# Performance work log

Measured on AMD Instinct MI355X. Metric: run time of the kernel, lower is better.

The kernel has to match this reference:

```python
import jax, jax.numpy as jnp
import numpy as np

T = 2048          # sequence length
B = 1             # batch (forced by out.squeeze(1))
H = 2048          # hidden_size == input_size
L = 2             # num_layers
V = 128           # num_letters
TEMPERATURE = 1.0


def _lstm_layer(x, h0, c0, W_ih, W_hh, b_ih, b_hh):
    # x: [T, B, H_in], h0/c0: [B, H], W_ih: [4H, H_in], W_hh: [4H, H]
    b = b_ih + b_hh

    def step(carry, x_t):
        h, c = carry
        gates = x_t @ W_ih.T + h @ W_hh.T + b            # [B, 4H]
        i, f, g, o = jnp.split(gates, 4, axis=-1)        # torch gate order i,f,g,o
        i = jax.nn.sigmoid(i)
        f = jax.nn.sigmoid(f)
        g = jnp.tanh(g)
        o = jax.nn.sigmoid(o)
        c = f * c + i * g
        h = o * jnp.tanh(c)
        return (h, c), h

    (hT, cT), ys = jax.lax.scan(step, (h0, c0), x)       # ys: [T, B, H]
    return ys, hT, cT


def setup_inputs() -> dict:
    key = jax.random.key(0)
    ks = jax.random.split(key, 10)
    s = 1.0 / np.sqrt(H)  # torch default uniform init bound
    u = lambda k, shape: jax.random.uniform(k, shape, jnp.float32, -s, s)
    return {
        "x": jax.random.normal(ks[0], (T, B, H), jnp.float32),
        "h0": jnp.zeros((L, B, H), jnp.float32),
        "c0": jnp.zeros((L, B, H), jnp.float32),
        "W_ih": u(ks[1], (L, 4 * H, H)),
        "W_hh": u(ks[2], (L, 4 * H, H)),
        "b_ih": u(ks[3], (L, 4 * H)),
        "b_hh": u(ks[4], (L, 4 * H)),
        "fc_w": u(ks[5], (V, H)),
        "fc_b": u(ks[6], (V,)),
    }


def reference(x, h0, c0, W_ih, W_hh, b_ih, b_hh, fc_w, fc_b):
    out = x
    h_n, c_n = [], []
    for l in range(L):  # fixed small layer loop (dropout=0.1 is identity in eval)
        out, hT, cT = _lstm_layer(out, h0[l], c0[l], W_ih[l], W_hh[l], b_ih[l], b_hh[l])
        h_n.append(hT)
        c_n.append(cT)
    h_n = jnp.stack(h_n)
    c_n = jnp.stack(c_n)
    logits = out[:, 0, :] @ fc_w.T + fc_b                 # squeeze(1) -> [T, V]
    logp = jax.nn.log_softmax(logits / TEMPERATURE, axis=1)
    return logp, (h_n, c_n)
```

## Files before the change

### kernel.cpp

```cpp
#include <hip/hip_runtime.h>
#include <hip/hip_fp16.h>

#define T_LEN 2048
#define HID   2048
#define G4    8192
#define NV    128

typedef _Float16 h2_t __attribute__((ext_vector_type(2)));
typedef unsigned u32x4 __attribute__((ext_vector_type(4)));

__device__ __forceinline__ float uplo(unsigned u) {
  return __half2float(__ushort_as_half((unsigned short)(u & 0xffffu)));
}
__device__ __forceinline__ float uphi(unsigned u) {
  return __half2float(__ushort_as_half((unsigned short)(u >> 16)));
}
__device__ __forceinline__ unsigned pku(float a, float b) {
  unsigned lo = (unsigned)__half_as_ushort(__float2half_rn(a));
  unsigned hi = (unsigned)__half_as_ushort(__float2half_rn(b));
  return lo | (hi << 16);
}
__device__ __forceinline__ h2_t pk2(float a, float bb) {
  return __builtin_bit_cast(h2_t, __builtin_amdgcn_cvt_pkrtz(a, bb));
}

__device__ __forceinline__ uint4 ld_sc16(const unsigned* p) {
  uint4 r;
  asm volatile("global_load_dwordx4 %0, %1, off sc0 sc1\n\ts_waitcnt vmcnt(0)"
               : "=v"(r) : "v"(p) : "memory");
  return r;
}
__device__ __forceinline__ void st_sc16(unsigned* p, u32x4 v) {
  asm volatile("global_store_dwordx4 %0, %1, off sc0 sc1\n\ts_waitcnt vmcnt(0)"
               :: "v"(p), "v"(v) : "memory");
}
__device__ __forceinline__ void st_sc4(unsigned* p, unsigned v) {
  asm volatile("global_store_dword %0, %1, off sc0 sc1"
               :: "v"(p), "v"(v) : "memory");
}

__device__ __forceinline__ float fsigmoid(float x) {
  return __builtin_amdgcn_rcpf(1.f + __expf(-x));
}
__device__ __forceinline__ float ftanh(float x) {
  return 2.f * __builtin_amdgcn_rcpf(1.f + __expf(-2.f * x)) - 1.f;
}

__device__ __forceinline__ void poll_flags(const unsigned* f, unsigned want,
                                           int lane) {
  const unsigned* p = f + 4 * lane;
  int sp = 0;
  for (;;) {
    uint4 u = ld_sc16(p);
    bool ok = (u.x == want) & (u.y == want) & (u.z == want) & (u.w == want);
    if (__all(ok)) break;
    if (++sp > 8) __builtin_amdgcn_s_sleep(1);
    if (sp > (1 << 15)) break;
  }
}

__global__ __launch_bounds__(256) void zero_flags(unsigned* f, int n4) {
  u32x4 z = {0u, 0u, 0u, 0u};
  for (int i = blockIdx.x * 256 + threadIdx.x; i < n4; i += gridDim.x * 256)
    st_sc16(f + 4 * (size_t)i, z);
}

__global__ __launch_bounds__(256, 2) void gemm_bias(
    const float* __restrict__ A, const float* __restrict__ B,
    const float* __restrict__ b1, const float* __restrict__ b2,
    float* __restrict__ C)
{
  const int N = 8192, K = 2048;
  __shared__ float As[32][68];
  __shared__ float Bs[32][68];
  const int tid = threadIdx.x;
  const int tx = tid & 15, ty = tid >> 4;
  const int row0 = blockIdx.y * 64, col0 = blockIdx.x * 64;
  const int lk = (tid & 7) * 4, lr = tid >> 3;
  float acc[4][4] = {};
  for (int k0 = 0; k0 < K; k0 += 32) {
    float4 a0 = *(const float4*)&A[(size_t)(row0 + lr)      * K + k0 + lk];
    float4 a1 = *(const float4*)&A[(size_t)(row0 + lr + 32) * K + k0 + lk];
    float4 bb0 = *(const float4*)&B[(size_t)(col0 + lr)      * K + k0 + lk];
    float4 bb1 = *(const float4*)&B[(size_t)(col0 + lr + 32) * K + k0 + lk];
    __syncthreads();
    As[lk+0][lr] = a0.x;  As[lk+1][lr] = a0.y;  As[lk+2][lr] = a0.z;  As[lk+3][lr] = a0.w;
    As[lk+0][lr+32] = a1.x; As[lk+1][lr+32] = a1.y; As[lk+2][lr+32] = a1.z; As[lk+3][lr+32] = a1.w;
    Bs[lk+0][lr] = bb0.x; Bs[lk+1][lr] = bb0.y; Bs[lk+2][lr] = bb0.z; Bs[lk+3][lr] = bb0.w;
    Bs[lk+0][lr+32] = bb1.x; Bs[lk+1][lr+32] = bb1.y; Bs[lk+2][lr+32] = bb1.z; Bs[lk+3][lr+32] = bb1.w;
    __syncthreads();
    #pragma unroll
    for (int kk = 0; kk < 32; ++kk) {
      float4 av = *(const float4*)&As[kk][ty * 4];
      float4 bv = *(const float4*)&Bs[kk][tx * 4];
      float am[4] = {av.x, av.y, av.z, av.w};
      float bm[4] = {bv.x, bv.y, bv.z, bv.w};
      #pragma unroll
      for (int i = 0; i < 4; ++i)
        #pragma unroll
        for (int j = 0; j < 4; ++j)
          acc[i][j] = fmaf(am[i], bm[j], acc[i][j]);
    }
  }
  #pragma unroll
  for (int i = 0; i < 4; ++i) {
    const int r = row0 + ty * 4 + i;
    #pragma unroll
    for (int j = 0; j < 4; ++j) {
      const int cc = col0 + tx * 4 + j;
      C[(size_t)r * N + cc] = acc[i][j] + b1[cc] + b2[cc];
    }
  }
}

__global__ __launch_bounds__(512) void lstm_rec2(
    const float* __restrict__ Whh0,
    const float* __restrict__ Wih1,
    const float* __restrict__ Whh1,
    const float* __restrict__ G,
    const float* __restrict__ bih1, const float* __restrict__ bhh1,
    const float* __restrict__ h0v,
    const float* __restrict__ c0v,
    unsigned* Hrow0, unsigned* Hrow1,
    unsigned* flags0, unsigned* flags1,
    float* __restrict__ hn, float* __restrict__ cn)
{
  const int b = blockIdx.x;
  const int tid = threadIdx.x;
  const int w = tid >> 6;
  const int lane = tid & 63;
  const int j = b * 8 + w;
  __shared__ unsigned hs0[2][HID / 2];
  __shared__ unsigned hs1[2][HID / 2];
  __shared__ float hloc0[8], hloc1[8];

  h2_t wreg0[4][16], wregI[4][16], wregH[4][16];
  #pragma unroll
  for (int g = 0; g < 4; ++g) {
    const float* r0 = Whh0 + (size_t)(g * 2048 + j) * 2048 + 2 * lane;
    #pragma unroll
    for (int it = 0; it < 16; ++it) {
      float2 v = *(const float2*)(r0 + 128 * it);
      wreg0[g][it] = pk2(v.x, v.y);
    }
  }
  #pragma unroll
  for (int g = 0; g < 4; ++g) {
    const float* rI = Wih1 + (size_t)(g * 2048 + j) * 2048 + 2 * lane;
    #pragma unroll
    for (int it = 0; it < 16; ++it) {
      float2 v = *(const float2*)(rI + 128 * it);
      wregI[g][it] = pk2(v.x, v.y);
    }
  }
  #pragma unroll
  for (int g = 0; g < 4; ++g) {
    const float* rH = Whh1 + (size_t)(g * 2048 + j) * 2048 + 2 * lane;
    #pragma unroll
    for (int it = 0; it < 16; ++it) {
      float2 v = *(const float2*)(rH + 128 * it);
      wregH[g][it] = pk2(v.x, v.y);
    }
  }
  float bias1[4];
  #pragma unroll
  for (int g = 0; g < 4; ++g)
    bias1[g] = bih1[g * 2048 + j] + bhh1[g * 2048 + j];

  float c0val = c0v[j];
  float c1val = c0v[HID + j];
  float h0last = 0.f, h1last = 0.f;

  if (tid == 0) {
    u32x4 P = {pku(h0v[b*8+0], h0v[b*8+1]),
               pku(h0v[b*8+2], h0v[b*8+3]),
               pku(h0v[b*8+4], h0v[b*8+5]),
               pku(h0v[b*8+6], h0v[b*8+7])};
    st_sc16(Hrow0 + b * 4, P);
    st_sc4(flags0 + b, 1u);
  }
  if (tid == 64) {
    u32x4 P = {pku(h0v[HID+b*8+0], h0v[HID+b*8+1]),
               pku(h0v[HID+b*8+2], h0v[HID+b*8+3]),
               pku(h0v[HID+b*8+4], h0v[HID+b*8+5]),
               pku(h0v[HID+b*8+6], h0v[HID+b*8+7])};
    st_sc16(Hrow1 + b * 4, P);
    st_sc4(flags1 + b, 1u);
  }

  for (int r = 1; r <= T_LEN + 1; ++r) {
    const bool doL0 = (r <= T_LEN);
    const bool doL1 = (r >= 2);
    float gpre = (doL0 && lane < 4) ? G[(size_t)(r - 1) * G4 + lane * 2048 + j] : 0.f;

    if (w == 0)        poll_flags(flags0 + (size_t)(r - 1) * 256, (unsigned)r, lane);
    else if (w == 1 && doL1) poll_flags(flags1 + (size_t)(r - 2) * 256, (unsigned)(r - 1), lane);
    __syncthreads();

    if (tid < 256) {
      uint4 u = ld_sc16(Hrow0 + (size_t)(r - 1) * 1024 + 4 * tid);
      *(uint4*)&hs0[r & 1][4 * tid] = u;
    } else if (doL1) {
      const int q = tid - 256;
      uint4 u = ld_sc16(Hrow1 + (size_t)(r - 2) * 1024 + 4 * q);
      *(uint4*)&hs1[r & 1][4 * q] = u;
    }
    __syncthreads();

    if (doL0) {
      const unsigned* hr = hs0[r & 1];
      float a0 = 0.f, a1 = 0.f, a2 = 0.f, a3 = 0.f;
      #pragma unroll
      for (int it = 0; it < 16; ++it) {
        h2_t hv = __builtin_bit_cast(h2_t, hr[lane + 64 * it]);
        a0 = __builtin_amdgcn_fdot2(wreg0[0][it], hv, a0, false);
        a1 = __builtin_amdgcn_fdot2(wreg0[1][it], hv, a1, false);
        a2 = __builtin_amdgcn_fdot2(wreg0[2][it], hv, a2, false);
        a3 = __builtin_amdgcn_fdot2(wreg0[3][it], hv, a3, false);
      }
      #pragma unroll
      for (int off = 32; off > 0; off >>= 1) {
        a0 += __shfl_xor(a0, off, 64);
        a1 += __shfl_xor(a1, off, 64);
        a2 += __shfl_xor(a2, off, 64);
        a3 += __shfl_xor(a3, off, 64);
      }
      float g0 = __shfl(gpre, 0, 64), g1 = __shfl(gpre, 1, 64);
      float g2 = __shfl(gpre, 2, 64), g3 = __shfl(gpre, 3, 64);
      float ig = fsigmoid(a0 + g0);
      float fg = fsigmoid(a1 + g1);
      float gg = ftanh(a2 + g2);
      float og = fsigmoid(a3 + g3);
      c0val = fg * c0val + ig * gg;
      h0last = og * ftanh(c0val);
      if (lane == 0) hloc0[w] = h0last;
    }
    __syncthreads();
    if (doL0 && tid == 0) {
      u32x4 P = {pku(hloc0[0], hloc0[1]), pku(hloc0[2], hloc0[3]),
                 pku(hloc0[4], hloc0[5]), pku(hloc0[6], hloc0[7])};
      st_sc16(Hrow0 + (size_t)r * 1024 + b * 4, P);
      st_sc4(flags0 + (size_t)r * 256 + b, (unsigned)(r + 1));
    }

    if (doL1) {
      const unsigned* xr = hs0[r & 1];
      const unsigned* hr = hs1[r & 1];
      float a0 = 0.f, a1 = 0.f, a2 = 0.f, a3 = 0.f;
      #pragma unroll
      for (int it = 0; it < 16; ++it) {
        h2_t xv = __builtin_bit_cast(h2_t, xr[lane + 64 * it]);
        a0 = __builtin_amdgcn_fdot2(wregI[0][it], xv, a0, false);
        a1 = __builtin_amdgcn_fdot2(wregI[1][it], xv, a1, false);
        a2 = __builtin_amdgcn_fdot2(wregI[2][it], xv, a2, false);
        a3 = __builtin_amdgcn_fdot2(wregI[3][it], xv, a3, false);
        h2_t hv = __builtin_bit_cast(h2_t, hr[lane + 64 * it]);
        a0 = __builtin_amdgcn_fdot2(wregH[0][it], hv, a0, false);
        a1 = __builtin_amdgcn_fdot2(wregH[1][it], hv, a1, false);
        a2 = __builtin_amdgcn_fdot2(wregH[2][it], hv, a2, false);
        a3 = __builtin_amdgcn_fdot2(wregH[3][it], hv, a3, false);
      }
      #pragma unroll
      for (int off = 32; off > 0; off >>= 1) {
        a0 += __shfl_xor(a0, off, 64);
        a1 += __shfl_xor(a1, off, 64);
        a2 += __shfl_xor(a2, off, 64);
        a3 += __shfl_xor(a3, off, 64);
      }
      float ig = fsigmoid(a0 + bias1[0]);
      float fg = fsigmoid(a1 + bias1[1]);
      float gg = ftanh(a2 + bias1[2]);
      float og = fsigmoid(a3 + bias1[3]);
      c1val = fg * c1val + ig * gg;
      h1last = og * ftanh(c1val);
      if (lane == 0) hloc1[w] = h1last;
    }
    __syncthreads();
    if (doL1 && tid == 64) {
      u32x4 P = {pku(hloc1[0], hloc1[1]), pku(hloc1[2], hloc1[3]),
                 pku(hloc1[4], hloc1[5]), pku(hloc1[6], hloc1[7])};
      st_sc16(Hrow1 + (size_t)(r - 1) * 1024 + b * 4, P);
      st_sc4(flags1 + (size_t)(r - 1) * 256 + b, (unsigned)r);
    }
  }
  if (lane == 0) {
    hn[j] = h0last;       cn[j] = c0val;
    hn[HID + j] = h1last; cn[HID + j] = c1val;
  }
}

__global__ __launch_bounds__(128) void fc_lsm(
    const unsigned* __restrict__ Hrows,
    const float* __restrict__ fcw,
    const float* __restrict__ fcb,
    float* __restrict__ out)
{
  const int t = blockIdx.x;
  const int v = threadIdx.x;
  __shared__ float hs[HID];
  __shared__ float red[4];
  const unsigned* hrow = Hrows + (size_t)t * 1024;
  for (int q = v; q < 256; q += 128) {
    uint4 uv = *(const uint4*)&hrow[q * 4];
    hs[q*8+0] = uplo(uv.x); hs[q*8+1] = uphi(uv.x);
    hs[q*8+2] = uplo(uv.y); hs[q*8+3] = uphi(uv.y);
    hs[q*8+4] = uplo(uv.z); hs[q*8+5] = uphi(uv.z);
    hs[q*8+6] = uplo(uv.w); hs[q*8+7] = uphi(uv.w);
  }
  __syncthreads();
  const float* wrow = fcw + (size_t)v * HID;
  float acc = fcb[v];
  #pragma unroll 4
  for (int k = 0; k < HID; k += 4) {
    float4 wv = *(const float4*)&wrow[k];
    acc = fmaf(wv.x, hs[k],     acc);
    acc = fmaf(wv.y, hs[k + 1], acc);
    acc = fmaf(wv.z, hs[k + 2], acc);
    acc = fmaf(wv.w, hs[k + 3], acc);
  }
  float m = acc;
  #pragma unroll
  for (int off = 32; off > 0; off >>= 1) m = fmaxf(m, __shfl_xor(m, off, 64));
  if ((v & 63) == 0) red[v >> 6] = m;
  __syncthreads();
  m = fmaxf(red[0], red[1]);
  float e = expf(acc - m), s = e;
  #pragma unroll
  for (int off = 32; off > 0; off >>= 1) s += __shfl_xor(s, off, 64);
  if ((v & 63) == 0) red[2 + (v >> 6)] = s;
  __syncthreads();
  s = red[2] + red[3];
  out[(size_t)t * NV + v] = (acc - m) - logf(s);
}

extern "C" void kernel_launch(void* const* d_in, const int* in_sizes, int n_in,
                              void* d_out, int out_size, void* d_ws, size_t ws_size,
                              hipStream_t stream) {
  const float* x   = (const float*)d_in[0];
  const float* h0  = (const float*)d_in[1];
  const float* c0  = (const float*)d_in[2];
  const float* Wih = (const float*)d_in[3];
  const float* Whh = (const float*)d_in[4];
  const float* bih = (const float*)d_in[5];
  const float* bhh = (const float*)d_in[6];
  const float* fcw = (const float*)d_in[7];
  const float* fcb = (const float*)d_in[8];
  float* out = (float*)d_out;

  char* ws = (char*)d_ws;
  float*    G      = (float*)(ws);
  unsigned* Hrow0  = (unsigned*)(ws + 67108864);
  unsigned* Hrow1  = (unsigned*)(ws + 67108864 + 8392704);
  unsigned* flags0 = (unsigned*)(ws + 67108864 + 2 * 8392704);
  unsigned* flags1 = (unsigned*)(ws + 67108864 + 2 * 8392704 + 2098176);

  const int nflag4 = (2 * 2098176) / 16;
  zero_flags<<<256, 256, 0, stream>>>(flags0, nflag4);

  dim3 ggrid(G4 / 64, T_LEN / 64);

  gemm_bias<<<ggrid, 256, 0, stream>>>(x, Wih, bih, bhh, G);
  lstm_rec2<<<256, 512, 0, stream>>>(Whh, Wih + (size_t)G4 * HID,
                                     Whh + (size_t)G4 * HID, G,
                                     bih + G4, bhh + G4, h0, c0,
                                     Hrow0, Hrow1, flags0, flags1,
                                     out + 262144, out + 266240);
  fc_lsm<<<T_LEN, 128, 0, stream>>>(Hrow1 + 1024, fcw, fcb, out);
}
```

Before: 13.43 ms.

## Replace flag arrays with self-validating fp16 hidden rows and pack gate precompute

Removes the separate flag arrays and the per-step block barriers plus leader stores. Each wave now writes its own fp16 h value directly, encoded so that zero is never written, and consumers poll the data rows until every halfword is nonzero. The input-projection GEMM now writes its bias-added output packed as fp16, which halves the precompute buffer and the per-step loads. In exchange it adds an encoding tweak (exact zero becomes the smallest denormal), keeps the input GEMM output at fp16 precision, and relies on 2-byte stores being seen as complete within 16-byte polled loads.

```diff
diff --git a/kernel.cpp b/kernel.cpp
--- a/kernel.cpp
+++ b/kernel.cpp
@@ -7,7 +7,7 @@
 #define NV    128
 
 typedef _Float16 h2_t __attribute__((ext_vector_type(2)));
-typedef unsigned u32x4 __attribute__((ext_vector_type(4)));
+typedef unsigned short u16;
 
 __device__ __forceinline__ float uplo(unsigned u) {
   return __half2float(__ushort_as_half((unsigned short)(u & 0xffffu)));
@@ -22,6 +22,13 @@
 }
 __device__ __forceinline__ h2_t pk2(float a, float bb) {
   return __builtin_bit_cast(h2_t, __builtin_amdgcn_cvt_pkrtz(a, bb));
+}
+__device__ __forceinline__ h2_t bc2(unsigned u) {
+  return __builtin_bit_cast(h2_t, u);
+}
+__device__ __forceinline__ unsigned enc16(float h) {
+  unsigned u = (unsigned)__half_as_ushort(__float2half_rn(h));
+  return u ? u : 1u;
 }
 
 __device__ __forceinline__ uint4 ld_sc16(const unsigned* p) {
@@ -30,12 +37,13 @@
                : "=v"(r) : "v"(p) : "memory");
   return r;
 }
+__device__ __forceinline__ void st_sc2(u16* p, unsigned v) {
+  asm volatile("global_store_short %0, %1, off sc0 sc1"
+               :: "v"(p), "v"(v) : "memory");
+}
+typedef unsigned u32x4 __attribute__((ext_vector_type(4)));
 __device__ __forceinline__ void st_sc16(unsigned* p, u32x4 v) {
-  asm volatile("global_store_dwordx4 %0, %1, off sc0 sc1\n\ts_waitcnt vmcnt(0)"
-               :: "v"(p), "v"(v) : "memory");
-}
-__device__ __forceinline__ void st_sc4(unsigned* p, unsigned v) {
-  asm volatile("global_store_dword %0, %1, off sc0 sc1"
+  asm volatile("global_store_dwordx4 %0, %1, off sc0 sc1"
                :: "v"(p), "v"(v) : "memory");
 }
 
@@ -46,31 +54,18 @@
   return 2.f * __builtin_amdgcn_rcpf(1.f + __expf(-2.f * x)) - 1.f;
 }
 
-__device__ __forceinline__ void poll_flags(const unsigned* f, unsigned want,
-                                           int lane) {
-  const unsigned* p = f + 4 * lane;
-  int sp = 0;
-  for (;;) {
-    uint4 u = ld_sc16(p);
-    bool ok = (u.x == want) & (u.y == want) & (u.z == want) & (u.w == want);
-    if (__all(ok)) break;
-    if (++sp > 8) __builtin_amdgcn_s_sleep(1);
-    if (sp > (1 << 15)) break;
-  }
-}
-
-__global__ __launch_bounds__(256) void zero_flags(unsigned* f, int n4) {
+__global__ __launch_bounds__(256) void zero_rows(unsigned* f, int n4) {
   u32x4 z = {0u, 0u, 0u, 0u};
   for (int i = blockIdx.x * 256 + threadIdx.x; i < n4; i += gridDim.x * 256)
     st_sc16(f + 4 * (size_t)i, z);
 }
 
-__global__ __launch_bounds__(256, 2) void gemm_bias(
+__global__ __launch_bounds__(256, 2) void gemm_bias_pk(
     const float* __restrict__ A, const float* __restrict__ B,
     const float* __restrict__ b1, const float* __restrict__ b2,
-    float* __restrict__ C)
+    unsigned* __restrict__ Gp)
 {
-  const int N = 8192, K = 2048;
+  const int K = 2048;
   __shared__ float As[32][68];
   __shared__ float Bs[32][68];
   const int tid = threadIdx.x;
@@ -102,27 +97,29 @@
           acc[i][j] = fmaf(am[i], bm[j], acc[i][j]);
     }
   }
+  const int cc = col0 + tx * 4;
+  const float bbv0 = b1[cc+0] + b2[cc+0];
+  const float bbv1 = b1[cc+1] + b2[cc+1];
+  const float bbv2 = b1[cc+2] + b2[cc+2];
+  const float bbv3 = b1[cc+3] + b2[cc+3];
   #pragma unroll
   for (int i = 0; i < 4; ++i) {
     const int r = row0 + ty * 4 + i;
-    #pragma unroll
-    for (int j = 0; j < 4; ++j) {
-      const int cc = col0 + tx * 4 + j;
-      C[(size_t)r * N + cc] = acc[i][j] + b1[cc] + b2[cc];
-    }
-  }
-}
-
-__global__ __launch_bounds__(512) void lstm_rec2(
+    unsigned* gp = Gp + (size_t)r * (G4 / 2) + (cc >> 1);
+    gp[0] = pku(acc[i][0] + bbv0, acc[i][1] + bbv1);
+    gp[1] = pku(acc[i][2] + bbv2, acc[i][3] + bbv3);
+  }
+}
+
+__global__ __launch_bounds__(512, 2) void lstm_rec2(
     const float* __restrict__ Whh0,
     const float* __restrict__ Wih1,
     const float* __restrict__ Whh1,
-    const float* __restrict__ G,
+    const unsigned* __restrict__ Gp,
     const float* __restrict__ bih1, const float* __restrict__ bhh1,
     const float* __restrict__ h0v,
     const float* __restrict__ c0v,
-    unsigned* Hrow0, unsigned* Hrow1,
-    unsigned* flags0, unsigned* flags1,
+    u16* Hrow0, u16* Hrow1,
     float* __restrict__ hn, float* __restrict__ cn)
 {
   const int b = blockIdx.x;
@@ -132,7 +129,6 @@
   const int j = b * 8 + w;
   __shared__ unsigned hs0[2][HID / 2];
   __shared__ unsigned hs1[2][HID / 2];
-  __shared__ float hloc0[8], hloc1[8];
 
   h2_t wreg0[4][16], wregI[4][16], wregH[4][16];
   #pragma unroll
@@ -171,39 +167,50 @@
   float c1val = c0v[HID + j];
   float h0last = 0.f, h1last = 0.f;
 
-  if (tid == 0) {
-    u32x4 P = {pku(h0v[b*8+0], h0v[b*8+1]),
-               pku(h0v[b*8+2], h0v[b*8+3]),
-               pku(h0v[b*8+4], h0v[b*8+5]),
-               pku(h0v[b*8+6], h0v[b*8+7])};
-    st_sc16(Hrow0 + b * 4, P);
-    st_sc4(flags0 + b, 1u);
-  }
-  if (tid == 64) {
-    u32x4 P = {pku(h0v[HID+b*8+0], h0v[HID+b*8+1]),
-               pku(h0v[HID+b*8+2], h0v[HID+b*8+3]),
-               pku(h0v[HID+b*8+4], h0v[HID+b*8+5]),
-               pku(h0v[HID+b*8+6], h0v[HID+b*8+7])};
-    st_sc16(Hrow1 + b * 4, P);
-    st_sc4(flags1 + b, 1u);
-  }
+  if (lane == 0) {
+    st_sc2(Hrow0 + j, enc16(h0v[j]));
+    st_sc2(Hrow1 + j, enc16(h0v[HID + j]));
+  }
+
+  const unsigned* H0_32 = (const unsigned*)Hrow0;
+  const unsigned* H1_32 = (const unsigned*)Hrow1;
 
   for (int r = 1; r <= T_LEN + 1; ++r) {
     const bool doL0 = (r <= T_LEN);
     const bool doL1 = (r >= 2);
-    float gpre = (doL0 && lane < 4) ? G[(size_t)(r - 1) * G4 + lane * 2048 + j] : 0.f;
-
-    if (w == 0)        poll_flags(flags0 + (size_t)(r - 1) * 256, (unsigned)r, lane);
-    else if (w == 1 && doL1) poll_flags(flags1 + (size_t)(r - 2) * 256, (unsigned)(r - 1), lane);
-    __syncthreads();
+    unsigned gpre = 0;
+    if (doL0 && lane < 4)
+      gpre = Gp[(size_t)(r - 1) * (G4 / 2) + lane * 1024 + (j >> 1)];
 
     if (tid < 256) {
-      uint4 u = ld_sc16(Hrow0 + (size_t)(r - 1) * 1024 + 4 * tid);
-      *(uint4*)&hs0[r & 1][4 * tid] = u;
+      const unsigned* src = H0_32 + (size_t)(r - 1) * 1024 + 4 * tid;
+      uint4 u;
+      int sp = 0;
+      for (;;) {
+        u = ld_sc16(src);
+        bool ok = (u.x & 0xffffu) && (u.x >> 16) && (u.y & 0xffffu) && (u.y >> 16) &&
+                  (u.z & 0xffffu) && (u.z >> 16) && (u.w & 0xffffu) && (u.w >> 16);
+        if (ok) break;
+        if (++sp > 4) __builtin_amdgcn_s_sleep(1);
+        if (sp > (1 << 15)) break;
+      }
+      unsigned* d = &hs0[r & 1][4 * tid];
+      d[0] = u.x; d[1] = u.y; d[2] = u.z; d[3] = u.w;
     } else if (doL1) {
       const int q = tid - 256;
-      uint4 u = ld_sc16(Hrow1 + (size_t)(r - 2) * 1024 + 4 * q);
-      *(uint4*)&hs1[r & 1][4 * q] = u;
+      const unsigned* src = H1_32 + (size_t)(r - 2) * 1024 + 4 * q;
+      uint4 u;
+      int sp = 0;
+      for (;;) {
+        u = ld_sc16(src);
+        bool ok = (u.x & 0xffffu) && (u.x >> 16) && (u.y & 0xffffu) && (u.y >> 16) &&
+                  (u.z & 0xffffu) && (u.z >> 16) && (u.w & 0xffffu) && (u.w >> 16);
+        if (ok) break;
+        if (++sp > 4) __builtin_amdgcn_s_sleep(1);
+        if (sp > (1 << 15)) break;
+      }
+      unsigned* d = &hs1[r & 1][4 * q];
+      d[0] = u.x; d[1] = u.y; d[2] = u.z; d[3] = u.w;
     }
     __syncthreads();
 
@@ -212,7 +219,7 @@
       float a0 = 0.f, a1 = 0.f, a2 = 0.f, a3 = 0.f;
       #pragma unroll
       for (int it = 0; it < 16; ++it) {
-        h2_t hv = __builtin_bit_cast(h2_t, hr[lane + 64 * it]);
+        h2_t hv = bc2(hr[lane + 64 * it]);
         a0 = __builtin_amdgcn_fdot2(wreg0[0][it], hv, a0, false);
         a1 = __builtin_amdgcn_fdot2(wreg0[1][it], hv, a1, false);
         a2 = __builtin_amdgcn_fdot2(wreg0[2][it], hv, a2, false);
@@ -225,22 +232,21 @@
         a2 += __shfl_xor(a2, off, 64);
         a3 += __shfl_xor(a3, off, 64);
       }
-      float g0 = __shfl(gpre, 0, 64), g1 = __shfl(gpre, 1, 64);
-      float g2 = __shfl(gpre, 2, 64), g3 = __shfl(gpre, 3, 64);
+      unsigned gu0 = __shfl(gpre, 0, 64), gu1 = __shfl(gpre, 1, 64);
+      unsigned gu2 = __shfl(gpre, 2, 64), gu3 = __shfl(gpre, 3, 64);
+      const bool hi = (j & 1);
+      float g0 = hi ? uphi(gu0) : uplo(gu0);
+      float g1 = hi ? uphi(gu1) : uplo(gu1);
+      float g2 = hi ? uphi(gu2) : uplo(gu2);
+      float g3 = hi ? uphi(gu3) : uplo(gu3);
       float ig = fsigmoid(a0 + g0);
       float fg = fsigmoid(a1 + g1);
       float gg = ftanh(a2 + g2);
       float og = fsigmoid(a3 + g3);
       c0val = fg * c0val + ig * gg;
       h0last = og * ftanh(c0val);
-      if (lane == 0) hloc0[w] = h0last;
-    }
-    __syncthreads();
-    if (doL0 && tid == 0) {
-      u32x4 P = {pku(hloc0[0], hloc0[1]), pku(hloc0[2], hloc0[3]),
-                 pku(hloc0[4], hloc0[5]), pku(hloc0[6], hloc0[7])};
-      st_sc16(Hrow0 + (size_t)r * 1024 + b * 4, P);
-      st_sc4(flags0 + (size_t)r * 256 + b, (unsigned)(r + 1));
+      if (lane == 0)
+        st_sc2(Hrow0 + (size_t)r * HID + j, enc16(h0last));
     }
 
     if (doL1) {
@@ -249,12 +255,12 @@
       float a0 = 0.f, a1 = 0.f, a2 = 0.f, a3 = 0.f;
       #pragma unroll
       for (int it = 0; it < 16; ++it) {
-        h2_t xv = __builtin_bit_cast(h2_t, xr[lane + 64 * it]);
+        h2_t xv = bc2(xr[lane + 64 * it]);
         a0 = __builtin_amdgcn_fdot2(wregI[0][it], xv, a0, false);
         a1 = __builtin_amdgcn_fdot2(wregI[1][it], xv, a1, false);
         a2 = __builtin_amdgcn_fdot2(wregI[2][it], xv, a2, false);
         a3 = __builtin_amdgcn_fdot2(wregI[3][it], xv, a3, false);
-        h2_t hv = __builtin_bit_cast(h2_t, hr[lane + 64 * it]);
+        h2_t hv = bc2(hr[lane + 64 * it]);
         a0 = __builtin_amdgcn_fdot2(wregH[0][it], hv, a0, false);
         a1 = __builtin_amdgcn_fdot2(wregH[1][it], hv, a1, false);
         a2 = __builtin_amdgcn_fdot2(wregH[2][it], hv, a2, false);
@@ -273,14 +279,8 @@
       float og = fsigmoid(a3 + bias1[3]);
       c1val = fg * c1val + ig * gg;
       h1last = og * ftanh(c1val);
-      if (lane == 0) hloc1[w] = h1last;
-    }
-    __syncthreads();
-    if (doL1 && tid == 64) {
-      u32x4 P = {pku(hloc1[0], hloc1[1]), pku(hloc1[2], hloc1[3]),
-                 pku(hloc1[4], hloc1[5]), pku(hloc1[6], hloc1[7])};
-      st_sc16(Hrow1 + (size_t)(r - 1) * 1024 + b * 4, P);
-      st_sc4(flags1 + (size_t)(r - 1) * 256 + b, (unsigned)r);
+      if (lane == 0)
+        st_sc2(Hrow1 + (size_t)(r - 1) * HID + j, enc16(h1last));
     }
   }
   if (lane == 0) {
@@ -290,7 +290,7 @@
 }
 
 __global__ __launch_bounds__(128) void fc_lsm(
-    const unsigned* __restrict__ Hrows,
+    const u16* __restrict__ Hrows,
     const float* __restrict__ fcw,
     const float* __restrict__ fcb,
     float* __restrict__ out)
@@ -299,7 +299,7 @@
   const int v = threadIdx.x;
   __shared__ float hs[HID];
   __shared__ float red[4];
-  const unsigned* hrow = Hrows + (size_t)t * 1024;
+  const unsigned* hrow = (const unsigned*)(Hrows + (size_t)t * HID);
   for (int q = v; q < 256; q += 128) {
     uint4 uv = *(const uint4*)&hrow[q * 4];
     hs[q*8+0] = uplo(uv.x); hs[q*8+1] = uphi(uv.x);
@@ -348,22 +348,20 @@
   float* out = (float*)d_out;
 
   char* ws = (char*)d_ws;
-  float*    G      = (float*)(ws);
-  unsigned* Hrow0  = (unsigned*)(ws + 67108864);
-  unsigned* Hrow1  = (unsigned*)(ws + 67108864 + 8392704);
-  unsigned* flags0 = (unsigned*)(ws + 67108864 + 2 * 8392704);
-  unsigned* flags1 = (unsigned*)(ws + 67108864 + 2 * 8392704 + 2098176);
-
-  const int nflag4 = (2 * 2098176) / 16;
-  zero_flags<<<256, 256, 0, stream>>>(flags0, nflag4);
+  unsigned* Gp    = (unsigned*)(ws);
+  u16*      Hrow0 = (u16*)(ws + 33554432);
+  u16*      Hrow1 = (u16*)(ws + 33554432 + 8392704);
+
+  const int nrow4 = (2 * 8392704) / 16;
+  zero_rows<<<512, 256, 0, stream>>>((unsigned*)Hrow0, nrow4);
 
   dim3 ggrid(G4 / 64, T_LEN / 64);
 
-  gemm_bias<<<ggrid, 256, 0, stream>>>(x, Wih, bih, bhh, G);
+  gemm_bias_pk<<<ggrid, 256, 0, stream>>>(x, Wih, bih, bhh, Gp);
   lstm_rec2<<<256, 512, 0, stream>>>(Whh, Wih + (size_t)G4 * HID,
-                                     Whh + (size_t)G4 * HID, G,
+                                     Whh + (size_t)G4 * HID, Gp,
                                      bih + G4, bhh + G4, h0, c0,
-                                     Hrow0, Hrow1, flags0, flags1,
+                                     Hrow0, Hrow1,
                                      out + 262144, out + 266240);
-  fc_lsm<<<T_LEN, 128, 0, stream>>>(Hrow1 + 1024, fcw, fcb, out);
-}
+  fc_lsm<<<T_LEN, 128, 0, stream>>>(Hrow1 + HID, fcw, fcb, out);
+}
```

New measurement: 13.80 ms. +2.8%, slower.
